# Kernel optimization log

Measured on AMD Instinct MI355X. Metric: run time of the kernel, lower is better.

## Reference

```python
import math
import jax, jax.numpy as jnp
import numpy as np

DIM = 1024
DIM_QK = 128
DIM_V = 1024
CHUNK = 512
NUM_BUCKETS = 32
MAX_DISTANCE = 128


def _rel_pos_bucket(n_q, n_k):
    # causal T5 bucketing on the chunk-local grid
    q_pos = jnp.arange(n_q, dtype=jnp.int32)
    k_pos = jnp.arange(n_k, dtype=jnp.int32)
    rel = k_pos[None, :] - q_pos[:, None]          # [i, j]
    n = jnp.maximum(-rel, 0)                        # distance into the past
    max_exact = NUM_BUCKETS // 2
    is_small = n < max_exact
    n_f = jnp.maximum(n, 1).astype(jnp.float32)     # safe log
    val_large = max_exact + jnp.log(n_f / max_exact) / math.log(MAX_DISTANCE / max_exact) * (NUM_BUCKETS - max_exact)
    val_large = jnp.minimum(val_large, NUM_BUCKETS - 1)
    bucket = jnp.where(is_small, n.astype(jnp.float32), val_large)
    return bucket.astype(jnp.int32)                 # [i, j]


def setup_inputs() -> dict:
    key = jax.random.key(0)
    ks = jax.random.split(key, 6)
    b, s = 8, 4096
    x = jax.random.normal(ks[0], (b, s, DIM), dtype=jnp.float32)
    # Dense(dim_qk) / Dense(dim_value) params (glorot-ish scale)
    Wqk = jax.random.normal(ks[1], (DIM, DIM_QK), dtype=jnp.float32) * (1.0 / math.sqrt(DIM))
    bqk = jnp.zeros((DIM_QK,), dtype=jnp.float32)
    Wv = jax.random.normal(ks[2], (DIM, DIM_V), dtype=jnp.float32) * (1.0 / math.sqrt(DIM))
    bv = jnp.zeros((DIM_V,), dtype=jnp.float32)
    # OffsetScale: gamma ~ N(0, 0.02), beta = 0, heads=2
    gamma = jax.random.normal(ks[3], (2, DIM_QK), dtype=jnp.float32) * 0.02
    beta = jnp.zeros((2, DIM_QK), dtype=jnp.float32)
    # T5 relative position bias embedding table [num_buckets, 1]
    rel_emb = jax.random.normal(ks[4], (NUM_BUCKETS, 1), dtype=jnp.float32) * 0.05
    return {"x": x, "Wqk": Wqk, "bqk": bqk, "Wv": Wv, "bv": bv,
            "gamma": gamma, "beta": beta, "rel_emb": rel_emb}


def reference(x, Wqk, bqk, Wv, bv, gamma, beta, rel_emb):
    b, s, dim = x.shape
    qk = jax.nn.swish(x @ Wqk + bqk)                # [b, s, dqk]
    v = jax.nn.swish(x @ Wv + bv)                   # [b, s, dv]
    # OffsetScale with 2 heads -> q, k
    os = qk[..., None, :] * gamma + beta            # [b, s, 2, dqk]
    q, k = os[..., 0, :], os[..., 1, :]
    # chunk: [b, nk, c, z] (block-diagonal attention within chunks)
    c = CHUNK
    nk = s // c
    q = q.reshape(b, nk, c, DIM_QK)
    k = k.reshape(b, nk, c, DIM_QK)
    vc = v.reshape(b, nk, c, DIM_V)
    scale = dim ** (-0.5)                           # NOTE: input dim, faithful to source
    sim = jnp.einsum('bkiz,bkjz->bkij', q, k) * scale
    # T5 rel-pos bias on the chunk-local (c, c) grid, scaled by dim_qk ** 0.5
    bucket = _rel_pos_bucket(c, c)
    bias = rel_emb[bucket, 0] * (DIM_QK ** 0.5)     # [c, c]
    sim = sim + bias
    # causal mask: strictly-upper (future) positions -> -inf
    future = jnp.triu(jnp.ones((c, c), dtype=bool), k=1)
    sim = jnp.where(future, -jnp.inf, sim)
    attn = jax.nn.softmax(sim, axis=-1)
    out = jnp.einsum('bkij,bkjz->bkiz', attn, vc)
    return out.reshape(b, s, DIM_V)
```

## Files before the change

kernel.cpp:

```cpp
#include <hip/hip_runtime.h>
#include <hip/hip_bf16.h>

using bf16x8 = __attribute__((ext_vector_type(8))) short;
using f32x4  = __attribute__((ext_vector_type(4))) float;
typedef unsigned short u16;

#define SQRT128 11.313708498984761f

__device__ __forceinline__ u16 f2bf(float f) {
  unsigned u = __builtin_bit_cast(unsigned, f);
  u += 0x7fffu + ((u >> 16) & 1u);
  return (u16)(u >> 16);
}

__device__ __forceinline__ float swishf(float c) {
  return c / (1.0f + __expf(-c));
}

__device__ __forceinline__ void gld16(const void* g, void* l) {
  __builtin_amdgcn_global_load_lds((const __attribute__((address_space(1))) unsigned*)g,
                                   (__attribute__((address_space(3))) unsigned*)l, 16, 0, 0);
}

__global__ __launch_bounds__(256) void prep_xb(const float* __restrict__ x,
                                               u16* __restrict__ xb) {
  size_t t = ((size_t)blockIdx.x * 256 + threadIdx.x) * 8;
  float4 f0 = *(const float4*)(x + t);
  float4 f1 = *(const float4*)(x + t + 4);
  uint4 p;
  p.x = f2bf(f0.x) | ((unsigned)f2bf(f0.y) << 16);
  p.y = f2bf(f0.z) | ((unsigned)f2bf(f0.w) << 16);
  p.z = f2bf(f1.x) | ((unsigned)f2bf(f1.y) << 16);
  p.w = f2bf(f1.z) | ((unsigned)f2bf(f1.w) << 16);
  *(uint4*)(xb + t) = p;
}

__global__ __launch_bounds__(256) void prep_wqkt(const float* __restrict__ Wqk,
                                                 u16* __restrict__ Wqkt) {
  int t = blockIdx.x * 256 + threadIdx.x;
  int n = t >> 10, k = t & 1023;
  Wqkt[t] = f2bf(Wqk[(size_t)k * 128 + n]);
}

__global__ __launch_bounds__(256) void prep_wvt(const float* __restrict__ Wv,
                                                u16* __restrict__ Wvt) {
  int t = blockIdx.x * 256 + threadIdx.x;
  int n = t >> 10, k = t & 1023;
  Wvt[t] = f2bf(Wv[(size_t)k * 1024 + n]);
}

__global__ __launch_bounds__(512) void prep_bias(const float* __restrict__ rel_emb,
                                                 float* __restrict__ bias_tab) {
  int d = threadIdx.x;
  int b;
  if (d < 16) {
    b = d;
  } else {
    float v = 16.0f + __logf((float)d * 0.0625f) * (16.0f / 2.0794415416798357f);
    b = (int)v;
    if (b > 31) b = 31;
  }
  bias_tab[d] = rel_emb[b] * SQRT128;
}

__global__ __launch_bounds__(256, 2) void proj_kernel(
    const u16* __restrict__ xb,
    const u16* __restrict__ Wqkt, const u16* __restrict__ Wvt,
    const float* __restrict__ bqk, const float* __restrict__ bv,
    const float* __restrict__ gamma, const float* __restrict__ beta,
    u16* __restrict__ qm, u16* __restrict__ km, u16* __restrict__ vt) {
  __shared__ u16 a_lds[128 * 64];
  __shared__ u16 b_lds[128 * 64];
  const int tid = threadIdx.x;
  const int lane = tid & 63;
  const int w = tid >> 6;
  const int wm = w >> 1, wn = w & 1;
  const int nb = blockIdx.x;
  const int m0 = blockIdx.y * 128;
  const u16* Wt = (nb == 0) ? Wqkt : (Wvt + (size_t)(nb - 1) * 128 * 1024);

  f32x4 acc[4][4];
#pragma unroll
  for (int i = 0; i < 4; i++)
#pragma unroll
    for (int j = 0; j < 4; j++) acc[i][j] = f32x4{0.f, 0.f, 0.f, 0.f};

  const int srow_sub = w * 8 + (lane >> 3);
  const int sbyte = (lane & 7) * 16;

  for (int kt = 0; kt < 16; ++kt) {
    const int k0 = kt * 64;
    __syncthreads();
#pragma unroll
    for (int i = 0; i < 4; ++i) {
      const int row = i * 32 + srow_sub;
      const int colb = sbyte ^ ((row & 7) << 4);
      gld16(xb + (size_t)(m0 + row) * 1024 + k0 + (colb >> 1), &a_lds[(i * 4 + w) * 512]);
      gld16(Wt + (size_t)row * 1024 + k0 + (colb >> 1), &b_lds[(i * 4 + w) * 512]);
    }
    __syncthreads();
#pragma unroll
    for (int kk = 0; kk < 2; ++kk) {
      bf16x8 af[4], bfr[4];
#pragma unroll
      for (int mi = 0; mi < 4; mi++) {
        const int row = wm * 64 + mi * 16 + (lane & 15);
        const int byte_ = (kk * 64 + (lane >> 4) * 16) ^ ((row & 7) << 4);
        af[mi] = *(const bf16x8*)((const char*)a_lds + row * 128 + byte_);
      }
#pragma unroll
      for (int ni = 0; ni < 4; ni++) {
        const int row = wn * 64 + ni * 16 + (lane & 15);
        const int byte_ = (kk * 64 + (lane >> 4) * 16) ^ ((row & 7) << 4);
        bfr[ni] = *(const bf16x8*)((const char*)b_lds + row * 128 + byte_);
      }
#pragma unroll
      for (int mi = 0; mi < 4; mi++)
#pragma unroll
        for (int ni = 0; ni < 4; ni++)
          acc[mi][ni] = __builtin_amdgcn_mfma_f32_16x16x32_bf16(af[mi], bfr[ni], acc[mi][ni], 0, 0, 0);
    }
  }

  if (nb == 0) {
#pragma unroll
    for (int ni = 0; ni < 4; ni++) {
      const int nn = wn * 64 + ni * 16 + (lane & 15);
      const float bb = bqk[nn];
      const float g0 = gamma[nn], g1 = gamma[128 + nn];
      const float be0 = beta[nn], be1 = beta[128 + nn];
#pragma unroll
      for (int mi = 0; mi < 4; mi++) {
#pragma unroll
        for (int r = 0; r < 4; r++) {
          const int m = m0 + wm * 64 + mi * 16 + (lane >> 4) * 4 + r;
          const float s = swishf(acc[mi][ni][r] + bb);
          qm[(size_t)m * 128 + nn] = f2bf(s * g0 + be0);
          km[(size_t)m * 128 + nn] = f2bf(s * g1 + be1);
        }
      }
    }
  } else {
#pragma unroll
    for (int ni = 0; ni < 4; ni++) {
      const int z = (nb - 1) * 128 + wn * 64 + ni * 16 + (lane & 15);
      const float bb = bv[z];
#pragma unroll
      for (int mi = 0; mi < 4; mi++) {
        const int m = m0 + wm * 64 + mi * 16 + (lane >> 4) * 4;
        const int chunkid = m >> 9;
        const int j = m & 511;
        ushort4 pk;
        pk.x = f2bf(swishf(acc[mi][ni][0] + bb));
        pk.y = f2bf(swishf(acc[mi][ni][1] + bb));
        pk.z = f2bf(swishf(acc[mi][ni][2] + bb));
        pk.w = f2bf(swishf(acc[mi][ni][3] + bb));
        *(ushort4*)&vt[((size_t)chunkid * 1024 + z) * 512 + j] = pk;
      }
    }
  }
}

__global__ __launch_bounds__(256, 2) void score_kernel(
    const u16* __restrict__ qm, const u16* __restrict__ km,
    const float* __restrict__ bias_tab, u16* __restrict__ P) {
  __shared__ u16 k_lds[64][136];
  const int tid = threadIdx.x;
  const int lane = tid & 63;
  const int wid = tid >> 6;
  const int qt = blockIdx.x;
  const int ch = blockIdx.y;

  bf16x8 qf[4];
  {
    const int r = ch * 512 + qt * 64 + wid * 16 + (lane & 15);
    const u16* qp = qm + (size_t)r * 128 + 8 * (lane >> 4);
#pragma unroll
    for (int kk = 0; kk < 4; kk++) qf[kk] = *(const bf16x8*)(qp + kk * 32);
  }

  f32x4 acc[32];
#pragma unroll
  for (int i = 0; i < 32; i++) acc[i] = f32x4{0.f, 0.f, 0.f, 0.f};

  const int srow = tid >> 2;
  const int soff = (tid & 3) * 32;

#pragma unroll
  for (int kt = 0; kt < 8; ++kt) {
    if (kt <= qt) {
      __syncthreads();
      {
        const u16* src = km + (size_t)(ch * 512 + kt * 64 + srow) * 128 + soff;
        uint4 w0 = *(const uint4*)(src);
        uint4 w1 = *(const uint4*)(src + 8);
        uint4 w2 = *(const uint4*)(src + 16);
        uint4 w3 = *(const uint4*)(src + 24);
        *(uint4*)&k_lds[srow][soff] = w0;
        *(uint4*)&k_lds[srow][soff + 8] = w1;
        *(uint4*)&k_lds[srow][soff + 16] = w2;
        *(uint4*)&k_lds[srow][soff + 24] = w3;
      }
      __syncthreads();
#pragma unroll
      for (int jt = 0; jt < 4; jt++) {
#pragma unroll
        for (int kk = 0; kk < 4; kk++) {
          bf16x8 kf = *(const bf16x8*)&k_lds[jt * 16 + (lane & 15)][kk * 32 + 8 * (lane >> 4)];
          acc[kt * 4 + jt] =
              __builtin_amdgcn_mfma_f32_16x16x32_bf16(kf, qf[kk], acc[kt * 4 + jt], 0, 0, 0);
        }
      }
    }
  }

  const float scale = 0.03125f;
  const int i = qt * 64 + wid * 16 + (lane & 15);
  const int jb = (lane >> 4) * 4;
  const int nct = (qt + 1) * 4;

  float mx = -INFINITY;
#pragma unroll
  for (int ct = 0; ct < 32; ++ct) {
    if (ct < nct) {
#pragma unroll
      for (int r = 0; r < 4; r++) {
        const int j = ct * 16 + jb + r;
        float val = (j <= i) ? (acc[ct][r] * scale + bias_tab[i - j]) : -INFINITY;
        acc[ct][r] = val;
        mx = fmaxf(mx, val);
      }
    }
  }
  mx = fmaxf(mx, __shfl_xor(mx, 16));
  mx = fmaxf(mx, __shfl_xor(mx, 32));
  float sum = 0.f;
#pragma unroll
  for (int ct = 0; ct < 32; ++ct) {
    if (ct < nct) {
#pragma unroll
      for (int r = 0; r < 4; r++) {
        float e = __expf(acc[ct][r] - mx);
        acc[ct][r] = e;
        sum += e;
      }
    }
  }
  sum += __shfl_xor(sum, 16);
  sum += __shfl_xor(sum, 32);
  const float inv = 1.0f / sum;
  const size_t base = ((size_t)ch * 512 + i) * 512 + jb;
#pragma unroll
  for (int ct = 0; ct < 32; ++ct) {
    ushort4 pk;
    if (ct < nct) {
      pk.x = f2bf(acc[ct][0] * inv);
      pk.y = f2bf(acc[ct][1] * inv);
      pk.z = f2bf(acc[ct][2] * inv);
      pk.w = f2bf(acc[ct][3] * inv);
    } else {
      pk.x = pk.y = pk.z = pk.w = 0;
    }
    *(ushort4*)&P[base + ct * 16] = pk;
  }
}

__global__ __launch_bounds__(256, 2) void out_kernel(
    const u16* __restrict__ P, const u16* __restrict__ vt,
    float* __restrict__ out) {
  __shared__ u16 a_lds[128 * 64];
  __shared__ u16 b_lds[128 * 64];
  const int tid = threadIdx.x;
  const int lane = tid & 63;
  const int w = tid >> 6;
  const int wm = w >> 1, wn = w & 1;
  const int mb = blockIdx.x;
  const int nb = blockIdx.y;
  const int ch = blockIdx.z;
  const u16* Ab = P + (size_t)ch * 512 * 512 + (size_t)mb * 128 * 512;
  const u16* Bb = vt + (size_t)ch * 1024 * 512 + (size_t)nb * 128 * 512;

  f32x4 acc[4][4];
#pragma unroll
  for (int i = 0; i < 4; i++)
#pragma unroll
    for (int j = 0; j < 4; j++) acc[i][j] = f32x4{0.f, 0.f, 0.f, 0.f};

  const int srow_sub = w * 8 + (lane >> 3);
  const int sbyte = (lane & 7) * 16;
  const int kend = (mb + 1) * 2;

  for (int kt = 0; kt < kend; ++kt) {
    const int k0 = kt * 64;
    __syncthreads();
#pragma unroll
    for (int i = 0; i < 4; ++i) {
      const int row = i * 32 + srow_sub;
      const int colb = sbyte ^ ((row & 7) << 4);
      gld16(Ab + (size_t)row * 512 + k0 + (colb >> 1), &a_lds[(i * 4 + w) * 512]);
      gld16(Bb + (size_t)row * 512 + k0 + (colb >> 1), &b_lds[(i * 4 + w) * 512]);
    }
    __syncthreads();
#pragma unroll
    for (int kk = 0; kk < 2; ++kk) {
      bf16x8 af[4], bfr[4];
#pragma unroll
      for (int mi = 0; mi < 4; mi++) {
        const int row = wm * 64 + mi * 16 + (lane & 15);
        const int byte_ = (kk * 64 + (lane >> 4) * 16) ^ ((row & 7) << 4);
        af[mi] = *(const bf16x8*)((const char*)a_lds + row * 128 + byte_);
      }
#pragma unroll
      for (int ni = 0; ni < 4; ni++) {
        const int row = wn * 64 + ni * 16 + (lane & 15);
        const int byte_ = (kk * 64 + (lane >> 4) * 16) ^ ((row & 7) << 4);
        bfr[ni] = *(const bf16x8*)((const char*)b_lds + row * 128 + byte_);
      }
#pragma unroll
      for (int mi = 0; mi < 4; mi++)
#pragma unroll
        for (int ni = 0; ni < 4; ni++)
          acc[mi][ni] = __builtin_amdgcn_mfma_f32_16x16x32_bf16(af[mi], bfr[ni], acc[mi][ni], 0, 0, 0);
    }
  }

#pragma unroll
  for (int ni = 0; ni < 4; ni++) {
    const int z = nb * 128 + wn * 64 + ni * 16 + (lane & 15);
#pragma unroll
    for (int mi = 0; mi < 4; mi++) {
#pragma unroll
      for (int r = 0; r < 4; r++) {
        const int i = mb * 128 + wm * 64 + mi * 16 + (lane >> 4) * 4 + r;
        out[((size_t)ch * 512 + i) * 1024 + z] = acc[mi][ni][r];
      }
    }
  }
}

extern "C" void kernel_launch(void* const* d_in, const int* in_sizes, int n_in,
                              void* d_out, int out_size, void* d_ws, size_t ws_size,
                              hipStream_t stream) {
  const float* x = (const float*)d_in[0];
  const float* Wqk = (const float*)d_in[1];
  const float* bqk = (const float*)d_in[2];
  const float* Wv = (const float*)d_in[3];
  const float* bv = (const float*)d_in[4];
  const float* gamma = (const float*)d_in[5];
  const float* beta = (const float*)d_in[6];
  const float* rel_emb = (const float*)d_in[7];

  char* ws = (char*)d_ws;
  u16* Wqkt = (u16*)(ws + 0);
  u16* Wvt = (u16*)(ws + 262144);
  float* bias_tab = (float*)(ws + 2359296);
  u16* qm = (u16*)(ws + 2361344);
  u16* km = (u16*)(ws + 10749952);
  u16* vt = (u16*)(ws + 19138560);
  u16* P = (u16*)(ws + 86247424);
  float* out = (float*)d_out;
  u16* xb = (u16*)d_out;

  prep_xb<<<16384, 256, 0, stream>>>(x, xb);
  prep_wqkt<<<512, 256, 0, stream>>>(Wqk, Wqkt);
  prep_wvt<<<4096, 256, 0, stream>>>(Wv, Wvt);
  prep_bias<<<1, 512, 0, stream>>>(rel_emb, bias_tab);
  proj_kernel<<<dim3(9, 256), 256, 0, stream>>>(xb, Wqkt, Wvt, bqk, bv, gamma, beta, qm, km, vt);
  score_kernel<<<dim3(8, 64), 256, 0, stream>>>(qm, km, bias_tab, P);
  out_kernel<<<dim3(4, 8, 64), 256, 0, stream>>>(P, vt, out);
}
```

Before: 466.6 us.

## Fuse score and output kernels into one attention kernel, tile weight transposes

Merges score_kernel and out_kernel into a single attn_kernel. The kernel computes causal QK^T with the key tiles split across two wave groups, combines max and sum across the groups through LDS, keeps the softmax probabilities in LDS as bf16, and multiplies them with V streamed directly from global memory. This removes the global P write and read and one launch. The weight transpose prep kernels become an LDS-tiled transpose for coalesced access. Block indices for proj and attention are remapped so work is grouped by XCD and heavy and light query tiles alternate. In exchange the attention kernel runs one block of 512 threads with 64KB of LDS, and V is read without LDS staging, which may limit reuse and occupancy.

```diff
diff --git a/kernel.cpp b/kernel.cpp
--- a/kernel.cpp
+++ b/kernel.cpp
@@ -6,6 +6,7 @@
 typedef unsigned short u16;
 
 #define SQRT128 11.313708498984761f
+#define NINF (-__builtin_huge_valf())
 
 __device__ __forceinline__ u16 f2bf(float f) {
   unsigned u = __builtin_bit_cast(unsigned, f);
@@ -35,18 +36,27 @@
   *(uint4*)(xb + t) = p;
 }
 
-__global__ __launch_bounds__(256) void prep_wqkt(const float* __restrict__ Wqk,
-                                                 u16* __restrict__ Wqkt) {
-  int t = blockIdx.x * 256 + threadIdx.x;
-  int n = t >> 10, k = t & 1023;
-  Wqkt[t] = f2bf(Wqk[(size_t)k * 128 + n]);
-}
-
-__global__ __launch_bounds__(256) void prep_wvt(const float* __restrict__ Wv,
-                                                u16* __restrict__ Wvt) {
-  int t = blockIdx.x * 256 + threadIdx.x;
-  int n = t >> 10, k = t & 1023;
-  Wvt[t] = f2bf(Wv[(size_t)k * 1024 + n]);
+__global__ __launch_bounds__(256) void prep_wt(const float* __restrict__ W,
+                                               u16* __restrict__ Wt, int ncols) {
+  __shared__ float t[64][65];
+  const int tid = threadIdx.x;
+  const int k0 = blockIdx.x * 64, n0 = blockIdx.y * 64;
+#pragma unroll
+  for (int p = 0; p < 16; ++p) {
+    const int r = p * 4 + (tid >> 6);
+    const int c = tid & 63;
+    t[c][r] = W[(size_t)(k0 + r) * ncols + n0 + c];
+  }
+  __syncthreads();
+#pragma unroll
+  for (int p = 0; p < 8; ++p) {
+    const int n = p * 8 + (tid >> 5);
+    const int k2 = (tid & 31) * 2;
+    ushort2 pk;
+    pk.x = f2bf(t[n][k2]);
+    pk.y = f2bf(t[n][k2 + 1]);
+    *(ushort2*)&Wt[(size_t)(n0 + n) * 1024 + k0 + k2] = pk;
+  }
 }
 
 __global__ __launch_bounds__(512) void prep_bias(const float* __restrict__ rel_emb,
@@ -71,12 +81,17 @@
     u16* __restrict__ qm, u16* __restrict__ km, u16* __restrict__ vt) {
   __shared__ u16 a_lds[128 * 64];
   __shared__ u16 b_lds[128 * 64];
+  const int bid = blockIdx.x;
+  const int xcd = bid & 7;
+  const int s = bid >> 3;
+  const int mgrp = s / 9;
+  const int nb = s - mgrp * 9;
+  const int m0 = (mgrp * 8 + xcd) * 128;
+
   const int tid = threadIdx.x;
   const int lane = tid & 63;
   const int w = tid >> 6;
   const int wm = w >> 1, wn = w & 1;
-  const int nb = blockIdx.x;
-  const int m0 = blockIdx.y * 128;
   const u16* Wt = (nb == 0) ? Wqkt : (Wvt + (size_t)(nb - 1) * 128 * 1024);
 
   f32x4 acc[4][4];
@@ -134,9 +149,9 @@
 #pragma unroll
         for (int r = 0; r < 4; r++) {
           const int m = m0 + wm * 64 + mi * 16 + (lane >> 4) * 4 + r;
-          const float s = swishf(acc[mi][ni][r] + bb);
-          qm[(size_t)m * 128 + nn] = f2bf(s * g0 + be0);
-          km[(size_t)m * 128 + nn] = f2bf(s * g1 + be1);
+          const float sv = swishf(acc[mi][ni][r] + bb);
+          qm[(size_t)m * 128 + nn] = f2bf(sv * g0 + be0);
+          km[(size_t)m * 128 + nn] = f2bf(sv * g1 + be1);
         }
       }
     }
@@ -161,181 +176,178 @@
   }
 }
 
-__global__ __launch_bounds__(256, 2) void score_kernel(
+__global__ __launch_bounds__(512, 1) void attn_kernel(
     const u16* __restrict__ qm, const u16* __restrict__ km,
-    const float* __restrict__ bias_tab, u16* __restrict__ P) {
-  __shared__ u16 k_lds[64][136];
-  const int tid = threadIdx.x;
-  const int lane = tid & 63;
-  const int wid = tid >> 6;
-  const int qt = blockIdx.x;
-  const int ch = blockIdx.y;
-
-  bf16x8 qf[4];
-  {
-    const int r = ch * 512 + qt * 64 + wid * 16 + (lane & 15);
-    const u16* qp = qm + (size_t)r * 128 + 8 * (lane >> 4);
-#pragma unroll
-    for (int kk = 0; kk < 4; kk++) qf[kk] = *(const bf16x8*)(qp + kk * 32);
-  }
-
-  f32x4 acc[32];
-#pragma unroll
-  for (int i = 0; i < 32; i++) acc[i] = f32x4{0.f, 0.f, 0.f, 0.f};
-
-  const int srow = tid >> 2;
-  const int soff = (tid & 3) * 32;
-
-#pragma unroll
-  for (int kt = 0; kt < 8; ++kt) {
-    if (kt <= qt) {
-      __syncthreads();
-      {
-        const u16* src = km + (size_t)(ch * 512 + kt * 64 + srow) * 128 + soff;
-        uint4 w0 = *(const uint4*)(src);
-        uint4 w1 = *(const uint4*)(src + 8);
-        uint4 w2 = *(const uint4*)(src + 16);
-        uint4 w3 = *(const uint4*)(src + 24);
-        *(uint4*)&k_lds[srow][soff] = w0;
-        *(uint4*)&k_lds[srow][soff + 8] = w1;
-        *(uint4*)&k_lds[srow][soff + 16] = w2;
-        *(uint4*)&k_lds[srow][soff + 24] = w3;
-      }
-      __syncthreads();
-#pragma unroll
-      for (int jt = 0; jt < 4; jt++) {
-#pragma unroll
-        for (int kk = 0; kk < 4; kk++) {
-          bf16x8 kf = *(const bf16x8*)&k_lds[jt * 16 + (lane & 15)][kk * 32 + 8 * (lane >> 4)];
-          acc[kt * 4 + jt] =
-              __builtin_amdgcn_mfma_f32_16x16x32_bf16(kf, qf[kk], acc[kt * 4 + jt], 0, 0, 0);
-        }
-      }
-    }
-  }
-
-  const float scale = 0.03125f;
-  const int i = qt * 64 + wid * 16 + (lane & 15);
-  const int jb = (lane >> 4) * 4;
-  const int nct = (qt + 1) * 4;
-
-  float mx = -INFINITY;
-#pragma unroll
-  for (int ct = 0; ct < 32; ++ct) {
-    if (ct < nct) {
-#pragma unroll
-      for (int r = 0; r < 4; r++) {
-        const int j = ct * 16 + jb + r;
-        float val = (j <= i) ? (acc[ct][r] * scale + bias_tab[i - j]) : -INFINITY;
-        acc[ct][r] = val;
-        mx = fmaxf(mx, val);
-      }
-    }
-  }
-  mx = fmaxf(mx, __shfl_xor(mx, 16));
-  mx = fmaxf(mx, __shfl_xor(mx, 32));
-  float sum = 0.f;
-#pragma unroll
-  for (int ct = 0; ct < 32; ++ct) {
-    if (ct < nct) {
-#pragma unroll
-      for (int r = 0; r < 4; r++) {
-        float e = __expf(acc[ct][r] - mx);
-        acc[ct][r] = e;
-        sum += e;
-      }
-    }
-  }
-  sum += __shfl_xor(sum, 16);
-  sum += __shfl_xor(sum, 32);
-  const float inv = 1.0f / sum;
-  const size_t base = ((size_t)ch * 512 + i) * 512 + jb;
-#pragma unroll
-  for (int ct = 0; ct < 32; ++ct) {
-    ushort4 pk;
-    if (ct < nct) {
-      pk.x = f2bf(acc[ct][0] * inv);
-      pk.y = f2bf(acc[ct][1] * inv);
-      pk.z = f2bf(acc[ct][2] * inv);
-      pk.w = f2bf(acc[ct][3] * inv);
-    } else {
-      pk.x = pk.y = pk.z = pk.w = 0;
-    }
-    *(ushort4*)&P[base + ct * 16] = pk;
-  }
-}
-
-__global__ __launch_bounds__(256, 2) void out_kernel(
-    const u16* __restrict__ P, const u16* __restrict__ vt,
+    const u16* __restrict__ vt, const float* __restrict__ bias_tab,
     float* __restrict__ out) {
-  __shared__ u16 a_lds[128 * 64];
-  __shared__ u16 b_lds[128 * 64];
+  __shared__ char u_lds[65536];
+  __shared__ float mxbuf[2][64];
+  __shared__ float smbuf[2][64];
+  __shared__ float lds_bias[512];
+
+  const int bid = blockIdx.x;
+  const int xcd = bid & 7;
+  const int s = bid >> 3;
+  const int ch = (s >> 3) * 8 + xcd;
+  const int sq = s & 7;
+  const int qt = (sq & 1) ? (sq >> 1) : (7 - (sq >> 1));
+
   const int tid = threadIdx.x;
   const int lane = tid & 63;
   const int w = tid >> 6;
-  const int wm = w >> 1, wn = w & 1;
-  const int mb = blockIdx.x;
-  const int nb = blockIdx.y;
-  const int ch = blockIdx.z;
-  const u16* Ab = P + (size_t)ch * 512 * 512 + (size_t)mb * 128 * 512;
-  const u16* Bb = vt + (size_t)ch * 1024 * 512 + (size_t)nb * 128 * 512;
-
-  f32x4 acc[4][4];
+  const int g = lane >> 4;
+  const int l15 = lane & 15;
+  const int qg = w & 3;
+  const int kh = w >> 2;
+
+  lds_bias[tid] = bias_tab[tid];
+
+  const int qrow64 = qg * 16 + l15;
+  bf16x8 qf[4];
+  {
+    const u16* qp = qm + ((size_t)(ch * 512 + qt * 64 + qrow64)) * 128 + g * 8;
+#pragma unroll
+    for (int kk = 0; kk < 4; kk++) qf[kk] = *(const bf16x8*)(qp + kk * 32);
+  }
+
+  const int nt = qt + 1;
+  const int n0 = (nt + 1) >> 1;
+  const int myn = kh ? (nt - n0) : n0;
+
+  f32x4 acc[16];
+#pragma unroll
+  for (int i = 0; i < 16; i++) acc[i] = f32x4{0.f, 0.f, 0.f, 0.f};
+
+  for (int it = 0; it < n0; ++it) {
+    __syncthreads();
+#pragma unroll
+    for (int b = 0; b < 2; ++b) {
+      const int kt = b ? (n0 + it) : it;
+#pragma unroll
+      for (int i = 0; i < 2; ++i) {
+        const int slot = w * 2 + i;
+        const int r = slot * 4 + g;
+        const int colb = (l15 * 16) ^ ((r & 7) << 4);
+        gld16(km + ((size_t)(ch * 512 + kt * 64 + r)) * 128 + (colb >> 1),
+              u_lds + b * 16384 + slot * 1024);
+      }
+    }
+    __syncthreads();
+    if (!kh || it < nt - n0) {
+      const char* kb = u_lds + kh * 16384;
+#pragma unroll
+      for (int jt = 0; jt < 4; ++jt) {
+#pragma unroll
+        for (int kk = 0; kk < 4; ++kk) {
+          const int row = jt * 16 + l15;
+          bf16x8 kf = *(const bf16x8*)(kb + row * 256 + ((kk * 64 + g * 16) ^ ((row & 7) << 4)));
+          acc[it * 4 + jt] = __builtin_amdgcn_mfma_f32_16x16x32_bf16(kf, qf[kk], acc[it * 4 + jt], 0, 0, 0);
+        }
+      }
+    }
+  }
+
+  const float scale = 0.03125f;
+  const int ic = qt * 64 + qrow64;
+  float mx = NINF;
+#pragma unroll
+  for (int it = 0; it < 4; ++it) {
+    if (it < myn) {
+      const int kt = kh ? (n0 + it) : it;
+#pragma unroll
+      for (int jt = 0; jt < 4; ++jt) {
+#pragma unroll
+        for (int r = 0; r < 4; ++r) {
+          const int j = kt * 64 + jt * 16 + g * 4 + r;
+          int d = ic - j;
+          const float bv = lds_bias[d < 0 ? 0 : d];
+          const float val = (j <= ic) ? (acc[it * 4 + jt][r] * scale + bv) : NINF;
+          acc[it * 4 + jt][r] = val;
+          mx = fmaxf(mx, val);
+        }
+      }
+    }
+  }
+  mx = fmaxf(mx, __shfl_xor(mx, 16));
+  mx = fmaxf(mx, __shfl_xor(mx, 32));
+  if (g == 0) mxbuf[kh][qrow64] = mx;
+  __syncthreads();
+  const float M = fmaxf(mx, mxbuf[kh ^ 1][qrow64]);
+  float sum = 0.f;
+#pragma unroll
+  for (int it = 0; it < 4; ++it) {
+    if (it < myn) {
+#pragma unroll
+      for (int jt = 0; jt < 4; ++jt) {
+#pragma unroll
+        for (int r = 0; r < 4; ++r) {
+          const float e = __expf(acc[it * 4 + jt][r] - M);
+          acc[it * 4 + jt][r] = e;
+          sum += e;
+        }
+      }
+    }
+  }
+  sum += __shfl_xor(sum, 16);
+  sum += __shfl_xor(sum, 32);
+  if (g == 0) smbuf[kh][qrow64] = sum;
+  __syncthreads();
+  const float inv = 1.0f / (sum + smbuf[kh ^ 1][qrow64]);
+
+#pragma unroll
+  for (int it = 0; it < 4; ++it) {
+    if (it < myn) {
+      const int kt = kh ? (n0 + it) : it;
+      char* pt = u_lds + kt * 8192 + qrow64 * 128;
+#pragma unroll
+      for (int jt = 0; jt < 4; ++jt) {
+        ushort4 pk;
+        pk.x = f2bf(acc[it * 4 + jt][0] * inv);
+        pk.y = f2bf(acc[it * 4 + jt][1] * inv);
+        pk.z = f2bf(acc[it * 4 + jt][2] * inv);
+        pk.w = f2bf(acc[it * 4 + jt][3] * inv);
+        *(ushort4*)(pt + ((jt * 32 + g * 8) ^ ((qrow64 & 7) << 4))) = pk;
+      }
+    }
+  }
+  __syncthreads();
+
+  f32x4 oacc[4][8];
 #pragma unroll
   for (int i = 0; i < 4; i++)
 #pragma unroll
-    for (int j = 0; j < 4; j++) acc[i][j] = f32x4{0.f, 0.f, 0.f, 0.f};
-
-  const int srow_sub = w * 8 + (lane >> 3);
-  const int sbyte = (lane & 7) * 16;
-  const int kend = (mb + 1) * 2;
-
-  for (int kt = 0; kt < kend; ++kt) {
-    const int k0 = kt * 64;
-    __syncthreads();
-#pragma unroll
-    for (int i = 0; i < 4; ++i) {
-      const int row = i * 32 + srow_sub;
-      const int colb = sbyte ^ ((row & 7) << 4);
-      gld16(Ab + (size_t)row * 512 + k0 + (colb >> 1), &a_lds[(i * 4 + w) * 512]);
-      gld16(Bb + (size_t)row * 512 + k0 + (colb >> 1), &b_lds[(i * 4 + w) * 512]);
-    }
-    __syncthreads();
+    for (int j = 0; j < 8; j++) oacc[i][j] = f32x4{0.f, 0.f, 0.f, 0.f};
+  const int wcol = w * 128;
+
+  for (int kt = 0; kt <= qt; ++kt) {
+    const char* pt = u_lds + kt * 8192;
 #pragma unroll
     for (int kk = 0; kk < 2; ++kk) {
-      bf16x8 af[4], bfr[4];
-#pragma unroll
-      for (int mi = 0; mi < 4; mi++) {
-        const int row = wm * 64 + mi * 16 + (lane & 15);
-        const int byte_ = (kk * 64 + (lane >> 4) * 16) ^ ((row & 7) << 4);
-        af[mi] = *(const bf16x8*)((const char*)a_lds + row * 128 + byte_);
-      }
-#pragma unroll
-      for (int ni = 0; ni < 4; ni++) {
-        const int row = wn * 64 + ni * 16 + (lane & 15);
-        const int byte_ = (kk * 64 + (lane >> 4) * 16) ^ ((row & 7) << 4);
-        bfr[ni] = *(const bf16x8*)((const char*)b_lds + row * 128 + byte_);
-      }
-#pragma unroll
-      for (int mi = 0; mi < 4; mi++)
-#pragma unroll
-        for (int ni = 0; ni < 4; ni++)
-          acc[mi][ni] = __builtin_amdgcn_mfma_f32_16x16x32_bf16(af[mi], bfr[ni], acc[mi][ni], 0, 0, 0);
-    }
-  }
-
-#pragma unroll
-  for (int ni = 0; ni < 4; ni++) {
-    const int z = nb * 128 + wn * 64 + ni * 16 + (lane & 15);
-#pragma unroll
-    for (int mi = 0; mi < 4; mi++) {
-#pragma unroll
-      for (int r = 0; r < 4; r++) {
-        const int i = mb * 128 + wm * 64 + mi * 16 + (lane >> 4) * 4 + r;
-        out[((size_t)ch * 512 + i) * 1024 + z] = acc[mi][ni][r];
-      }
-    }
-  }
+      bf16x8 af[4];
+#pragma unroll
+      for (int mi = 0; mi < 4; ++mi) {
+        const int row = mi * 16 + l15;
+        af[mi] = *(const bf16x8*)(pt + row * 128 + ((kk * 64 + g * 16) ^ ((row & 7) << 4)));
+      }
+      const size_t kb = (size_t)kt * 64 + kk * 32 + g * 8;
+#pragma unroll
+      for (int ni = 0; ni < 8; ++ni) {
+        const bf16x8 bfr = *(const bf16x8*)(vt + ((size_t)ch * 1024 + wcol + ni * 16 + l15) * 512 + kb);
+#pragma unroll
+        for (int mi = 0; mi < 4; ++mi)
+          oacc[mi][ni] = __builtin_amdgcn_mfma_f32_16x16x32_bf16(af[mi], bfr, oacc[mi][ni], 0, 0, 0);
+      }
+    }
+  }
+
+  const size_t obase = (size_t)(ch * 512 + qt * 64) * 1024;
+#pragma unroll
+  for (int mi = 0; mi < 4; ++mi)
+#pragma unroll
+    for (int ni = 0; ni < 8; ++ni)
+#pragma unroll
+      for (int r = 0; r < 4; ++r)
+        out[obase + (size_t)(mi * 16 + g * 4 + r) * 1024 + wcol + ni * 16 + l15] = oacc[mi][ni][r];
 }
 
 extern "C" void kernel_launch(void* const* d_in, const int* in_sizes, int n_in,
@@ -357,15 +369,13 @@
   u16* qm = (u16*)(ws + 2361344);
   u16* km = (u16*)(ws + 10749952);
   u16* vt = (u16*)(ws + 19138560);
-  u16* P = (u16*)(ws + 86247424);
   float* out = (float*)d_out;
   u16* xb = (u16*)d_out;
 
   prep_xb<<<16384, 256, 0, stream>>>(x, xb);
-  prep_wqkt<<<512, 256, 0, stream>>>(Wqk, Wqkt);
-  prep_wvt<<<4096, 256, 0, stream>>>(Wv, Wvt);
+  prep_wt<<<dim3(16, 2), 256, 0, stream>>>(Wqk, Wqkt, 128);
+  prep_wt<<<dim3(16, 16), 256, 0, stream>>>(Wv, Wvt, 1024);
   prep_bias<<<1, 512, 0, stream>>>(rel_emb, bias_tab);
-  proj_kernel<<<dim3(9, 256), 256, 0, stream>>>(xb, Wqkt, Wvt, bqk, bv, gamma, beta, qm, km, vt);
-  score_kernel<<<dim3(8, 64), 256, 0, stream>>>(qm, km, bias_tab, P);
-  out_kernel<<<dim3(4, 8, 64), 256, 0, stream>>>(P, vt, out);
-}
+  proj_kernel<<<2304, 256, 0, stream>>>(xb, Wqkt, Wvt, bqk, bv, gamma, beta, qm, km, vt);
+  attn_kernel<<<512, 512, 0, stream>>>(qm, km, vt, bias_tab, out);
+}
```

Result: faster. 447.5 us (-4.1%).
